# Kernel tuning notes

Hardware: AMD Instinct MI355X
Metric: run time of the kernel (lower is better)

Reference implementation:

```python
import jax, jax.numpy as jnp
import numpy as np

T, B, D, H = 2048, 2, 1024, 16
DPH = D // H
SCALE = DPH ** -0.5


def setup_inputs() -> dict:
    key = jax.random.key(0)
    ks = jax.random.split(key, 5)
    x = jax.random.normal(ks[0], (T, B, D), dtype=jnp.float32)
    Wk = jax.random.normal(ks[1], (D, D), dtype=jnp.float32) * 0.02
    Wv = jax.random.normal(ks[2], (D, D), dtype=jnp.float32) * 0.02
    Wq = jax.random.normal(ks[3], (D, D), dtype=jnp.float32) * 0.02
    Wo = jax.random.normal(ks[4], (D, D), dtype=jnp.float32) * 0.02
    # causal mask: True marks positions to hide (masked_fill semantics)
    mask = jnp.triu(jnp.ones((T, T), dtype=bool), k=1)
    return {"x": x, "Wk": Wk, "Wv": Wv, "Wq": Wq, "Wo": Wo, "mask": mask}


def _split_heads(y):
    # 't b (d h) -> b h t d' : d_per_head is the OUTER factor of the split
    t, b, _ = y.shape
    return y.reshape(t, b, DPH, H).transpose(1, 3, 0, 2)  # [b, h, t, d]


def reference(x, Wk, Wv, Wq, Wo, mask):
    # nn.Linear(bias=False): y = x @ W.T
    k = _split_heads(x @ Wk.T)
    v = _split_heads(x @ Wv.T)
    q = _split_heads(x @ Wq.T)
    scores = jnp.einsum('bhid,bhjd->bhij', q, k) * SCALE  # [b,h,t,t]
    scores = jnp.where(mask, -jnp.inf, scores)
    attn = jax.nn.softmax(scores, axis=-1)
    # dropout is identity in eval mode
    out = jnp.einsum('bhij,bhjd->bhid', attn, v)  # [b,h,t,d]
    # 'b h t d -> t b (h d)' : heads are the OUTER factor of the merge
    out = out.transpose(2, 0, 1, 3).reshape(x.shape[0], x.shape[1], D)
    return out @ Wo.T
```

## Files before the change

kernel.cpp:

```cpp
#include <hip/hip_runtime.h>

#define T_LEN   2048
#define BATCH   2
#define DMODEL  1024
#define NHEAD   16
#define DHEAD   64
#define MROWS   4096
#define KDIM    1024
#define NDIM    1024
#define ATT_SC2 (0.125f * 1.44269504088896f)

typedef unsigned short u16;
typedef unsigned int   u32;
typedef u16   u16x8 __attribute__((ext_vector_type(8)));
typedef u16   u16x4 __attribute__((ext_vector_type(4)));
typedef __bf16 bf16x8 __attribute__((ext_vector_type(8)));
typedef float f32x4 __attribute__((ext_vector_type(4)));

__device__ __forceinline__ u16 f2bf(float f) {
  u32 u = __builtin_bit_cast(u32, f);
  u += 0x7fffu + ((u >> 16) & 1u);
  return (u16)(u >> 16);
}

__device__ __forceinline__ u16 bfc(float f) {
  return __builtin_bit_cast(u16, (__bf16)f);
}

__device__ __forceinline__ f32x4 mfma16(u16x8 a, u16x8 b, f32x4 c) {
  return __builtin_amdgcn_mfma_f32_16x16x32_bf16(
      __builtin_bit_cast(bf16x8, a), __builtin_bit_cast(bf16x8, b), c, 0, 0, 0);
}

__device__ __forceinline__ void gload16(const u16* g, u16* l) {
  __builtin_amdgcn_global_load_lds((const __attribute__((address_space(1))) void*)g,
                                   (__attribute__((address_space(3))) void*)l,
                                   16, 0, 0);
}

#define XN 4194304u
__global__ __launch_bounds__(256) void cast_all(
    const float* __restrict__ x,  const float* __restrict__ wk,
    const float* __restrict__ wv, const float* __restrict__ wq,
    const float* __restrict__ wo, u16* __restrict__ ws) {
  size_t i = ((size_t)blockIdx.x * 256 + threadIdx.x) * 4;
  const float* src; size_t soff, doff; float sc = 1.0f;
  if (i < XN) {
    int m = (int)(i >> 10), d = (int)(i & 1023);
    int t = m >> 1, b = m & 1;
    src = x; soff = i;
    doff = ((size_t)(b * 2048 + t) << 10) + d;
  } else {
    size_t off = i - XN;
    int wi = (int)(off >> 20);
    off &= 1048575u;
    int u = (int)(off >> 10), c = (int)(off & 1023);
    src = (wi == 0) ? wk : (wi == 1) ? wv : (wi == 2) ? wq : wo;
    soff = off;
    if (wi == 3) {
      doff = XN + 3u * 1048576u + off;
    } else {
      int slot = (wi == 2) ? 0 : (wi == 0) ? 1 : 2;
      int up = (u & 15) * 64 + (u >> 4);
      doff = XN + (size_t)slot * 1048576u + ((size_t)up << 10) + c;
      if (wi == 2) sc = ATT_SC2;
    }
  }
  float4 v = *reinterpret_cast<const float4*>(src + soff);
  u16x4 o;
  o.s0 = f2bf(v.x * sc); o.s1 = f2bf(v.y * sc); o.s2 = f2bf(v.z * sc); o.s3 = f2bf(v.w * sc);
  *reinterpret_cast<u16x4*>(ws + doff) = o;
}

__global__ __launch_bounds__(256, 2) void gemm_qkv(
    const u16* __restrict__ xbm, const u16* __restrict__ Wqkv,
    u16* __restrict__ Qh, u16* __restrict__ Kh, u16* __restrict__ Vt) {
  __shared__ __align__(16) u16 As[256 * 64];
  __shared__ __align__(16) u16 Bs[128 * 64];

  const int tid = threadIdx.x;
  const int l  = tid & 63, w = tid >> 6;
  const int lr = l & 15,  lg = l >> 4;
  const int wm = w >> 1,  wn = w & 1;

  const int blk  = blockIdx.x;
  const int wgid = (blk & 7) * 48 + (blk >> 3);

  const u16 *A, *W;
  int m0, n0, isV;
  if (wgid < 256) {
    const int bx = wgid >> 4, by = wgid & 15;
    A = xbm; W = Wqkv; m0 = by * 256; n0 = bx * 128; isV = 0;
  } else {
    const int v = wgid - 256;
    const int vby = v >> 5, vbx = v & 31;
    A = Wqkv + (2048u << 10); W = xbm; m0 = vby * 256; n0 = vbx * 128; isV = 1;
  }

  f32x4 acc[8][4];
#pragma unroll
  for (int i = 0; i < 8; ++i)
#pragma unroll
    for (int j = 0; j < 4; ++j) acc[i][j] = (f32x4)(0.0f);

  for (int k0 = 0; k0 < KDIM; k0 += 64) {
#pragma unroll
    for (int i = 0; i < 8; ++i) {
      const int base = i * 256 + w * 64;
      const int p = base + l;
      const int r = p >> 3, c = p & 7;
      gload16(A + (size_t)(m0 + r) * KDIM + k0 + ((c ^ (r & 7)) << 3),
              As + (size_t)base * 8);
    }
#pragma unroll
    for (int i = 0; i < 4; ++i) {
      const int base = i * 256 + w * 64;
      const int p = base + l;
      const int r = p >> 3, c = p & 7;
      gload16(W + (size_t)(n0 + r) * KDIM + k0 + ((c ^ (r & 7)) << 3),
              Bs + (size_t)base * 8);
    }
    __syncthreads();

#pragma unroll
    for (int ks = 0; ks < 2; ++ks) {
      const int cr = ks * 4 + lg;
      u16x8 bf_[4];
#pragma unroll
      for (int ni = 0; ni < 4; ++ni) {
        const int rr = wn * 64 + ni * 16 + lr;
        bf_[ni] = *reinterpret_cast<const u16x8*>(Bs + rr * 64 + ((cr ^ (rr & 7)) << 3));
      }
      __builtin_amdgcn_s_setprio(1);
#pragma unroll
      for (int mi = 0; mi < 8; ++mi) {
        const int rr = wm * 128 + mi * 16 + lr;
        const u16x8 af = *reinterpret_cast<const u16x8*>(
            As + rr * 64 + ((cr ^ (rr & 7)) << 3));
#pragma unroll
        for (int ni = 0; ni < 4; ++ni)
          acc[mi][ni] = mfma16(af, bf_[ni], acc[mi][ni]);
      }
      __builtin_amdgcn_s_setprio(0);
    }
    __syncthreads();
  }

#pragma unroll
  for (int mi = 0; mi < 8; ++mi)
#pragma unroll
    for (int ni = 0; ni < 4; ++ni)
#pragma unroll
      for (int r = 0; r < 4; ++r) {
        const int row = m0 + wm * 128 + mi * 16 + lg * 4 + r;
        const int col = n0 + wn * 64 + ni * 16 + lr;
        const u16 v = bfc(acc[mi][ni][r]);
        if (!isV) {
          const int bb = row >> 11, t = row & 2047;
          const int c = col & 1023, hh = c >> 6, dp = c & 63;
          u16* d = (col < 1024) ? Qh : Kh;
          d[(((size_t)(bb * NHEAD + hh) << 11) + t) * 64 + dp] = v;
        } else {
          const int hh = row >> 6, dp = row & 63;
          const int bb = col >> 11, t = col & 2047;
          Vt[((((size_t)(bb * NHEAD + hh)) * 64 + dp) << 11) + t] = v;
        }
      }
}

__global__ __launch_bounds__(256) void gemm_o(
    const u16* __restrict__ A, const u16* __restrict__ W, float* __restrict__ out) {
  __shared__ __align__(16) u16 As[128 * 64];
  __shared__ __align__(16) u16 Bs[64 * 64];

  const int tid = threadIdx.x;
  const int l  = tid & 63, w = tid >> 6;
  const int lr = l & 15,  lg = l >> 4;
  const int wm = w >> 1,  wn = w & 1;

  const int blk  = blockIdx.x;
  const int wgid = (blk & 7) * 64 + (blk >> 3);
  const int bx = wgid >> 5, by = wgid & 31;
  const int m0 = by * 128;
  const int n0 = bx * 64;

  f32x4 acc[4][2];
#pragma unroll
  for (int i = 0; i < 4; ++i)
#pragma unroll
    for (int j = 0; j < 2; ++j) acc[i][j] = (f32x4)(0.0f);

  for (int k0 = 0; k0 < KDIM; k0 += 64) {
#pragma unroll
    for (int i = 0; i < 4; ++i) {
      const int base = i * 256 + w * 64;
      const int p = base + l;
      const int r = p >> 3, c = p & 7;
      gload16(A + (size_t)(m0 + r) * KDIM + k0 + ((c ^ (r & 7)) << 3),
              As + (size_t)base * 8);
    }
#pragma unroll
    for (int i = 0; i < 2; ++i) {
      const int base = i * 256 + w * 64;
      const int p = base + l;
      const int r = p >> 3, c = p & 7;
      gload16(W + (size_t)(n0 + r) * KDIM + k0 + ((c ^ (r & 7)) << 3),
              Bs + (size_t)base * 8);
    }
    __syncthreads();

#pragma unroll
    for (int ks = 0; ks < 2; ++ks) {
      const int cr = ks * 4 + lg;
      u16x8 bf_[2];
#pragma unroll
      for (int ni = 0; ni < 2; ++ni) {
        const int rr = wn * 32 + ni * 16 + lr;
        bf_[ni] = *reinterpret_cast<const u16x8*>(Bs + rr * 64 + ((cr ^ (rr & 7)) << 3));
      }
      __builtin_amdgcn_s_setprio(1);
#pragma unroll
      for (int mi = 0; mi < 4; ++mi) {
        const int rr = wm * 64 + mi * 16 + lr;
        const u16x8 af = *reinterpret_cast<const u16x8*>(
            As + rr * 64 + ((cr ^ (rr & 7)) << 3));
#pragma unroll
        for (int ni = 0; ni < 2; ++ni)
          acc[mi][ni] = mfma16(af, bf_[ni], acc[mi][ni]);
      }
      __builtin_amdgcn_s_setprio(0);
    }
    __syncthreads();
  }

#pragma unroll
  for (int mi = 0; mi < 4; ++mi)
#pragma unroll
    for (int ni = 0; ni < 2; ++ni)
#pragma unroll
      for (int r = 0; r < 4; ++r) {
        const int row = m0 + wm * 64 + mi * 16 + lg * 4 + r;
        const int col = n0 + wn * 32 + ni * 16 + lr;
        const int t = row & 2047, bb = row >> 11;
        out[((size_t)(t * 2 + bb) << 10) + col] = acc[mi][ni][r];
      }
}

__global__ __launch_bounds__(256) void attn_fwd(
    const u16* __restrict__ Qh, const u16* __restrict__ Kh,
    const u16* __restrict__ Vt, u16* __restrict__ Aout) {
  __shared__ __align__(16) u16 Ks[2][8192];
  __shared__ __align__(16) u16 Vs[2][8192];
  __shared__ __align__(16) u16 Pl[4][1024];

  const int tid = threadIdx.x;
  const int l = tid & 63, w = tid >> 6;
  const int lr = l & 15, lg = l >> 4;
  const int blk = blockIdx.x;
  const int bxx = (blk >> 3) & 15;
  const int bh  = ((blk >> 7) << 3) + (blk & 7);
  const int b = bh >> 4, h = bh & 15;

  const u16* kg = Kh + ((size_t)bh << 17);
  const u16* vg = Vt + ((size_t)bh << 17);

  const u16x8 ones = {0x3F80,0x3F80,0x3F80,0x3F80,0x3F80,0x3F80,0x3F80,0x3F80};

  auto stage = [&](int buf, int kv0) {
#pragma unroll
    for (int j = 0; j < 4; ++j) {
      const int base = (j * 4 + w) * 64;
      const int g = base + l;
      const int rk = g >> 3, ck = g & 7;
      gload16(kg + (size_t)(kv0 + rk) * 64 + ((ck ^ (rk & 7)) << 3),
              &Ks[buf][(size_t)base * 8]);
      const int rv = g >> 4, cv = g & 15;
      gload16(vg + ((size_t)rv << 11) + kv0 + ((cv ^ (rv & 15)) << 3),
              &Vs[buf][(size_t)base * 8]);
    }
  };

  for (int ph = 0; ph < 2; ++ph) {
    const int qb = ph ? bxx : 31 - bxx;
    const int qbase = qb * 64 + w * 16;
    const int qrow = qbase + lr;

    const u16* qptr = Qh + (((size_t)bh << 11) + qrow) * 64 + lg * 8;
    const u16x8 qf0 = *reinterpret_cast<const u16x8*>(qptr);
    const u16x8 qf1 = *reinterpret_cast<const u16x8*>(qptr + 32);

    f32x4 oacc[4];
#pragma unroll
    for (int i = 0; i < 4; ++i) oacc[i] = (f32x4)(0.0f);
    f32x4 sum4 = (f32x4)(0.0f);

    const int npair = (qb + 2) >> 1;
    stage(0, 0);
    __syncthreads();

    int cur = 0;
    for (int t = 0; t < npair; ++t) {
      const int kv0 = t * 128;
      if (t + 1 < npair) stage(cur ^ 1, kv0 + 128);

#pragma unroll
      for (int hh = 0; hh < 2; ++hh) {
        const int i64 = 2 * t + hh;
        if (i64 <= qb) {
          const bool diag = (i64 == qb);

          __builtin_amdgcn_s_setprio(1);
#pragma unroll
          for (int tt = 0; tt < 4; ++tt) {
            const int row = hh * 64 + tt * 16 + lr;
            const u16x8 kf0 = *reinterpret_cast<const u16x8*>(
                &Ks[cur][row * 64 + ((lg ^ (row & 7)) << 3)]);
            const u16x8 kf1 = *reinterpret_cast<const u16x8*>(
                &Ks[cur][row * 64 + (((4 + lg) ^ (row & 7)) << 3)]);
            f32x4 sacc = (f32x4)(0.0f);
            sacc = mfma16(kf0, qf0, sacc);
            sacc = mfma16(kf1, qf1, sacc);
            u16x4 pk;
#pragma unroll
            for (int r = 0; r < 4; ++r) {
              const int kv = kv0 + hh * 64 + tt * 16 + lg * 4 + r;
              const float s = (diag && kv > qrow) ? -1e30f : sacc[r];
              pk[r] = bfc(__builtin_amdgcn_exp2f(s - 8.0f));
            }
            *reinterpret_cast<u16x4*>(
                &Pl[w][lr * 64 + (((tt * 2 + (lg >> 1)) ^ (lr & 7)) << 3)
                       + ((lg & 1) << 2)]) = pk;
          }

#pragma unroll
          for (int kh = 0; kh < 2; ++kh) {
            const u16x8 pa = *reinterpret_cast<const u16x8*>(
                &Pl[w][lr * 64 + (((kh * 4 + lg) ^ (lr & 7)) << 3)]);
            sum4 = mfma16(pa, ones, sum4);
#pragma unroll
            for (int ni = 0; ni < 4; ++ni) {
              const int dr = ni * 16 + lr;
              const int ck = hh * 8 + kh * 4 + lg;
              const u16x8 vf = *reinterpret_cast<const u16x8*>(
                  &Vs[cur][dr * 128 + ((ck ^ (dr & 15)) << 3)]);
              oacc[ni] = mfma16(pa, vf, oacc[ni]);
            }
          }
          __builtin_amdgcn_s_setprio(0);
        }
      }

      __syncthreads();
      cur ^= 1;
    }

#pragma unroll
    for (int r = 0; r < 4; ++r) {
      const float inv = 1.0f / sum4[r];
      const int q = qbase + lg * 4 + r;
      const size_t rowbase = (((size_t)(b * 2048 + q)) << 10) + h * DHEAD;
#pragma unroll
      for (int ni = 0; ni < 4; ++ni)
        Aout[rowbase + ni * 16 + lr] = bfc(oacc[ni][r] * inv);
    }
  }
}

extern "C" void kernel_launch(void* const* d_in, const int* in_sizes, int n_in,
                              void* d_out, int out_size, void* d_ws, size_t ws_size,
                              hipStream_t stream) {
  const float* x  = (const float*)d_in[0];
  const float* Wk = (const float*)d_in[1];
  const float* Wv = (const float*)d_in[2];
  const float* Wq = (const float*)d_in[3];
  const float* Wo = (const float*)d_in[4];

  u16* ws   = (u16*)d_ws;
  u16* xbm  = ws;
  u16* Wqkv = xbm + 4194304;
  u16* Wob  = Wqkv + 3145728;
  u16* Qh   = Wob + 1048576;
  u16* Kh   = Qh  + 4194304;
  u16* Vt   = Kh  + 4194304;
  u16* Aout = Vt  + 4194304;

  cast_all<<<8192, 256, 0, stream>>>(x, Wk, Wv, Wq, Wo, ws);

  gemm_qkv<<<384, 256, 0, stream>>>(xbm, Wqkv, Qh, Kh, Vt);

  attn_fwd<<<512, 256, 0, stream>>>(Qh, Kh, Vt, Aout);

  gemm_o<<<512, 256, 0, stream>>>(Aout, Wob, (float*)d_out);
}
```

Baseline: 111.3 us.

## Split attention KV tiles across warps and reduce partial outputs via shared memory

The attention kernel now gives each warp a 32-row slice of the 128-row KV tile for all four 16-row query groups, instead of one query group over the whole KV tile. K and V fragments are loaded from LDS once per warp and reused across query groups, and fully masked groups are skipped per warp. Per-warp partial outputs and row sums are then combined through shared memory at the end. This adds a cross-warp reduction, an extra barrier and more accumulator registers, and sets launch_bounds to 2 blocks per CU.

Result: slower. 165.9 us (+49.0%).

```diff
diff --git a/kernel.cpp b/kernel.cpp
--- a/kernel.cpp
+++ b/kernel.cpp
@@ -246,12 +246,10 @@
       }
 }
 
-__global__ __launch_bounds__(256) void attn_fwd(
+__global__ __launch_bounds__(256, 2) void attn_fwd(
     const u16* __restrict__ Qh, const u16* __restrict__ Kh,
     const u16* __restrict__ Vt, u16* __restrict__ Aout) {
-  __shared__ __align__(16) u16 Ks[2][8192];
-  __shared__ __align__(16) u16 Vs[2][8192];
-  __shared__ __align__(16) u16 Pl[4][1024];
+  __shared__ __align__(16) u16 smem[34816];
 
   const int tid = threadIdx.x;
   const int l = tid & 63, w = tid >> 6;
@@ -263,36 +261,45 @@
 
   const u16* kg = Kh + ((size_t)bh << 17);
   const u16* vg = Vt + ((size_t)bh << 17);
+  u16* Pw = smem + 32768 + w * 512;
 
   const u16x8 ones = {0x3F80,0x3F80,0x3F80,0x3F80,0x3F80,0x3F80,0x3F80,0x3F80};
 
   auto stage = [&](int buf, int kv0) {
+    u16* kb = smem + buf * 8192;
+    u16* vb = smem + 16384 + buf * 8192;
 #pragma unroll
     for (int j = 0; j < 4; ++j) {
       const int base = (j * 4 + w) * 64;
       const int g = base + l;
       const int rk = g >> 3, ck = g & 7;
       gload16(kg + (size_t)(kv0 + rk) * 64 + ((ck ^ (rk & 7)) << 3),
-              &Ks[buf][(size_t)base * 8]);
+              kb + (size_t)base * 8);
       const int rv = g >> 4, cv = g & 15;
       gload16(vg + ((size_t)rv << 11) + kv0 + ((cv ^ (rv & 15)) << 3),
-              &Vs[buf][(size_t)base * 8]);
+              vb + (size_t)base * 8);
     }
   };
 
   for (int ph = 0; ph < 2; ++ph) {
     const int qb = ph ? bxx : 31 - bxx;
-    const int qbase = qb * 64 + w * 16;
-    const int qrow = qbase + lr;
-
-    const u16* qptr = Qh + (((size_t)bh << 11) + qrow) * 64 + lg * 8;
-    const u16x8 qf0 = *reinterpret_cast<const u16x8*>(qptr);
-    const u16x8 qf1 = *reinterpret_cast<const u16x8*>(qptr + 32);
-
-    f32x4 oacc[4];
-#pragma unroll
-    for (int i = 0; i < 4; ++i) oacc[i] = (f32x4)(0.0f);
-    f32x4 sum4 = (f32x4)(0.0f);
+    const int qmax = qb * 64 + 63;
+
+    u16x8 qf[4][2];
+#pragma unroll
+    for (int qg = 0; qg < 4; ++qg) {
+      const int qrow = qb * 64 + qg * 16 + lr;
+      const u16* qptr = Qh + (((size_t)bh << 11) + qrow) * 64 + lg * 8;
+      qf[qg][0] = *reinterpret_cast<const u16x8*>(qptr);
+      qf[qg][1] = *reinterpret_cast<const u16x8*>(qptr + 32);
+    }
+
+    f32x4 oacc[4][4];
+#pragma unroll
+    for (int qg = 0; qg < 4; ++qg)
+#pragma unroll
+      for (int i = 0; i < 4; ++i) oacc[qg][i] = (f32x4)(0.0f);
+    f32x4 sum4[4] = {(f32x4)(0.0f), (f32x4)(0.0f), (f32x4)(0.0f), (f32x4)(0.0f)};
 
     const int npair = (qb + 2) >> 1;
     stage(0, 0);
@@ -303,50 +310,73 @@
       const int kv0 = t * 128;
       if (t + 1 < npair) stage(cur ^ 1, kv0 + 128);
 
-#pragma unroll
-      for (int hh = 0; hh < 2; ++hh) {
-        const int i64 = 2 * t + hh;
-        if (i64 <= qb) {
-          const bool diag = (i64 == qb);
-
-          __builtin_amdgcn_s_setprio(1);
-#pragma unroll
-          for (int tt = 0; tt < 4; ++tt) {
-            const int row = hh * 64 + tt * 16 + lr;
-            const u16x8 kf0 = *reinterpret_cast<const u16x8*>(
-                &Ks[cur][row * 64 + ((lg ^ (row & 7)) << 3)]);
-            const u16x8 kf1 = *reinterpret_cast<const u16x8*>(
-                &Ks[cur][row * 64 + (((4 + lg) ^ (row & 7)) << 3)]);
-            f32x4 sacc = (f32x4)(0.0f);
-            sacc = mfma16(kf0, qf0, sacc);
-            sacc = mfma16(kf1, qf1, sacc);
-            u16x4 pk;
-#pragma unroll
-            for (int r = 0; r < 4; ++r) {
-              const int kv = kv0 + hh * 64 + tt * 16 + lg * 4 + r;
-              const float s = (diag && kv > qrow) ? -1e30f : sacc[r];
-              pk[r] = bfc(__builtin_amdgcn_exp2f(s - 8.0f));
+      const int kvw = kv0 + w * 32;
+      if (kvw <= qmax) {
+        const u16* kb = smem + cur * 8192;
+        const u16* vb = smem + 16384 + cur * 8192;
+
+        u16x8 kf[2][2];
+#pragma unroll
+        for (int tt = 0; tt < 2; ++tt) {
+          const int row = w * 32 + tt * 16 + lr;
+          kf[tt][0] = *reinterpret_cast<const u16x8*>(
+              kb + row * 64 + ((lg ^ (row & 7)) << 3));
+          kf[tt][1] = *reinterpret_cast<const u16x8*>(
+              kb + row * 64 + (((4 + lg) ^ (row & 7)) << 3));
+        }
+        u16x8 vf[4];
+#pragma unroll
+        for (int ni = 0; ni < 4; ++ni) {
+          const int dr = ni * 16 + lr;
+          const int ck = w * 4 + lg;
+          vf[ni] = *reinterpret_cast<const u16x8*>(
+              vb + dr * 128 + ((ck ^ (dr & 15)) << 3));
+        }
+
+#pragma unroll
+        for (int qg = 0; qg < 4; ++qg) {
+          const int qbg = qb * 64 + qg * 16;
+          if (kvw <= qbg + 15) {
+            f32x4 s0 = (f32x4)(0.0f), s1 = (f32x4)(0.0f);
+            __builtin_amdgcn_s_setprio(1);
+            s0 = mfma16(kf[0][0], qf[qg][0], s0);
+            s0 = mfma16(kf[0][1], qf[qg][1], s0);
+            s1 = mfma16(kf[1][0], qf[qg][0], s1);
+            s1 = mfma16(kf[1][1], qf[qg][1], s1);
+            __builtin_amdgcn_s_setprio(0);
+
+            const int qrow = qbg + lr;
+            u16x4 pk0, pk1;
+            if (kvw + 31 > qbg) {
+#pragma unroll
+              for (int r = 0; r < 4; ++r) {
+                const int kva = kvw + lg * 4 + r;
+                pk0[r] = bfc(__builtin_amdgcn_exp2f(
+                    (kva > qrow ? -1e30f : s0[r]) - 8.0f));
+                pk1[r] = bfc(__builtin_amdgcn_exp2f(
+                    (kva + 16 > qrow ? -1e30f : s1[r]) - 8.0f));
+              }
+            } else {
+#pragma unroll
+              for (int r = 0; r < 4; ++r) {
+                pk0[r] = bfc(__builtin_amdgcn_exp2f(s0[r] - 8.0f));
+                pk1[r] = bfc(__builtin_amdgcn_exp2f(s1[r] - 8.0f));
+              }
             }
-            *reinterpret_cast<u16x4*>(
-                &Pl[w][lr * 64 + (((tt * 2 + (lg >> 1)) ^ (lr & 7)) << 3)
-                       + ((lg & 1) << 2)]) = pk;
+            const int wo0 = lr * 32 + ((((lg >> 1)) ^ (lr & 3)) << 3) + ((lg & 1) << 2);
+            const int wo1 = lr * 32 + (((2 + (lg >> 1)) ^ (lr & 3)) << 3) + ((lg & 1) << 2);
+            *reinterpret_cast<u16x4*>(Pw + wo0) = pk0;
+            *reinterpret_cast<u16x4*>(Pw + wo1) = pk1;
+
+            const u16x8 pa = *reinterpret_cast<const u16x8*>(
+                Pw + lr * 32 + ((lg ^ (lr & 3)) << 3));
+            __builtin_amdgcn_s_setprio(1);
+            sum4[qg] = mfma16(pa, ones, sum4[qg]);
+#pragma unroll
+            for (int ni = 0; ni < 4; ++ni)
+              oacc[qg][ni] = mfma16(pa, vf[ni], oacc[qg][ni]);
+            __builtin_amdgcn_s_setprio(0);
           }
-
-#pragma unroll
-          for (int kh = 0; kh < 2; ++kh) {
-            const u16x8 pa = *reinterpret_cast<const u16x8*>(
-                &Pl[w][lr * 64 + (((kh * 4 + lg) ^ (lr & 7)) << 3)]);
-            sum4 = mfma16(pa, ones, sum4);
-#pragma unroll
-            for (int ni = 0; ni < 4; ++ni) {
-              const int dr = ni * 16 + lr;
-              const int ck = hh * 8 + kh * 4 + lg;
-              const u16x8 vf = *reinterpret_cast<const u16x8*>(
-                  &Vs[cur][dr * 128 + ((ck ^ (dr & 15)) << 3)]);
-              oacc[ni] = mfma16(pa, vf, oacc[ni]);
-            }
-          }
-          __builtin_amdgcn_s_setprio(0);
         }
       }
 
@@ -354,15 +384,54 @@
       cur ^= 1;
     }
 
+    float* red  = reinterpret_cast<float*>(smem);
+    float* sred = reinterpret_cast<float*>(smem + 32768);
+#pragma unroll
+    for (int qg = 0; qg < 4; ++qg) {
+      if (qg != w) {
+        float* p = red + (qg * 4 + w) * 1024;
+#pragma unroll
+        for (int ni = 0; ni < 4; ++ni)
+#pragma unroll
+          for (int r = 0; r < 4; ++r)
+            p[(lg * 4 + r) * 64 + ni * 16 + lr] = oacc[qg][ni][r];
+        if (lr == 0) {
+#pragma unroll
+          for (int r = 0; r < 4; ++r)
+            sred[(qg * 4 + w) * 16 + lg * 4 + r] = sum4[qg][r];
+        }
+      }
+    }
+    __syncthreads();
+
+    f32x4 o_[4]; f32x4 ss = sum4[w];
+#pragma unroll
+    for (int ni = 0; ni < 4; ++ni) o_[ni] = oacc[w][ni];
+#pragma unroll
+    for (int src = 0; src < 4; ++src) {
+      if (src != w) {
+        const float* p = red + (w * 4 + src) * 1024;
+#pragma unroll
+        for (int ni = 0; ni < 4; ++ni)
+#pragma unroll
+          for (int r = 0; r < 4; ++r)
+            o_[ni][r] += p[(lg * 4 + r) * 64 + ni * 16 + lr];
+#pragma unroll
+        for (int r = 0; r < 4; ++r)
+          ss[r] += sred[(w * 4 + src) * 16 + lg * 4 + r];
+      }
+    }
+
 #pragma unroll
     for (int r = 0; r < 4; ++r) {
-      const float inv = 1.0f / sum4[r];
-      const int q = qbase + lg * 4 + r;
+      const float inv = 1.0f / ss[r];
+      const int q = qb * 64 + w * 16 + lg * 4 + r;
       const size_t rowbase = (((size_t)(b * 2048 + q)) << 10) + h * DHEAD;
 #pragma unroll
       for (int ni = 0; ni < 4; ++ni)
-        Aout[rowbase + ni * 16 + lr] = bfc(oacc[ni][r] * inv);
-    }
+        Aout[rowbase + ni * 16 + lr] = bfc(o_[ni][r] * inv);
+    }
+    __syncthreads();
   }
 }
 
```

## Split attention KV tiles across two waves per query slice with LDS reduction

Applied to the files above, without the earlier changes.

The attention kernel moves from 4 to 8 waves per block. Each pair of waves shares a 16-row query slice and splits every 64-wide KV tile into two 32-column halves, and the partial outputs and row sums are combined through LDS at the end. The KV tile shrinks from 128 to 64 columns, so shared memory per block drops. Synchronization switches to explicit vmcnt/lgkmcnt waits with raw barriers, and V fragments are loaded before the MFMAs. This aims to raise occupancy and latency hiding, at the cost of more barriers per KV element and an extra reduction step.

Measured after the change: 107.8 us. -3.2%, faster.

```diff
diff --git a/kernel.cpp b/kernel.cpp
--- a/kernel.cpp
+++ b/kernel.cpp
@@ -246,16 +246,15 @@
       }
 }
 
-__global__ __launch_bounds__(256) void attn_fwd(
+__global__ __launch_bounds__(512, 2) void attn_fwd(
     const u16* __restrict__ Qh, const u16* __restrict__ Kh,
     const u16* __restrict__ Vt, u16* __restrict__ Aout) {
-  __shared__ __align__(16) u16 Ks[2][8192];
-  __shared__ __align__(16) u16 Vs[2][8192];
-  __shared__ __align__(16) u16 Pl[4][1024];
+  __shared__ __align__(16) u16 smem[20480];
 
   const int tid = threadIdx.x;
   const int l = tid & 63, w = tid >> 6;
   const int lr = l & 15, lg = l >> 4;
+  const int wk = w & 1, wq = w >> 1;
   const int blk = blockIdx.x;
   const int bxx = (blk >> 3) & 15;
   const int bh  = ((blk >> 7) << 3) + (blk & 7);
@@ -263,27 +262,27 @@
 
   const u16* kg = Kh + ((size_t)bh << 17);
   const u16* vg = Vt + ((size_t)bh << 17);
+  u16* Pw = smem + 16384 + w * 512;
+
+  float* redO = reinterpret_cast<float*>(smem);
+  float* redS = reinterpret_cast<float*>(smem + 16384);
 
   const u16x8 ones = {0x3F80,0x3F80,0x3F80,0x3F80,0x3F80,0x3F80,0x3F80,0x3F80};
 
   auto stage = [&](int buf, int kv0) {
-#pragma unroll
-    for (int j = 0; j < 4; ++j) {
-      const int base = (j * 4 + w) * 64;
-      const int g = base + l;
-      const int rk = g >> 3, ck = g & 7;
-      gload16(kg + (size_t)(kv0 + rk) * 64 + ((ck ^ (rk & 7)) << 3),
-              &Ks[buf][(size_t)base * 8]);
-      const int rv = g >> 4, cv = g & 15;
-      gload16(vg + ((size_t)rv << 11) + kv0 + ((cv ^ (rv & 15)) << 3),
-              &Vs[buf][(size_t)base * 8]);
-    }
+    u16* kb = smem + buf * 4096;
+    u16* vb = smem + 8192 + buf * 4096;
+    const int p = w * 64 + l;
+    const int r = p >> 3, c = p & 7;
+    const int cs = ((c ^ (r & 7)) << 3);
+    gload16(kg + (size_t)(kv0 + r) * 64 + cs, kb + (size_t)(w * 64) * 8);
+    gload16(vg + ((size_t)r << 11) + kv0 + cs, vb + (size_t)(w * 64) * 8);
   };
 
   for (int ph = 0; ph < 2; ++ph) {
     const int qb = ph ? bxx : 31 - bxx;
-    const int qbase = qb * 64 + w * 16;
-    const int qrow = qbase + lr;
+    const int qbw = qb * 64 + wq * 16;
+    const int qrow = qbw + lr;
 
     const u16* qptr = Qh + (((size_t)bh << 11) + qrow) * 64 + lg * 8;
     const u16x8 qf0 = *reinterpret_cast<const u16x8*>(qptr);
@@ -294,75 +293,116 @@
     for (int i = 0; i < 4; ++i) oacc[i] = (f32x4)(0.0f);
     f32x4 sum4 = (f32x4)(0.0f);
 
-    const int npair = (qb + 2) >> 1;
+    const int nt = qb + 1;
     stage(0, 0);
     __syncthreads();
 
     int cur = 0;
-    for (int t = 0; t < npair; ++t) {
-      const int kv0 = t * 128;
-      if (t + 1 < npair) stage(cur ^ 1, kv0 + 128);
-
-#pragma unroll
-      for (int hh = 0; hh < 2; ++hh) {
-        const int i64 = 2 * t + hh;
-        if (i64 <= qb) {
-          const bool diag = (i64 == qb);
-
-          __builtin_amdgcn_s_setprio(1);
-#pragma unroll
-          for (int tt = 0; tt < 4; ++tt) {
-            const int row = hh * 64 + tt * 16 + lr;
-            const u16x8 kf0 = *reinterpret_cast<const u16x8*>(
-                &Ks[cur][row * 64 + ((lg ^ (row & 7)) << 3)]);
-            const u16x8 kf1 = *reinterpret_cast<const u16x8*>(
-                &Ks[cur][row * 64 + (((4 + lg) ^ (row & 7)) << 3)]);
-            f32x4 sacc = (f32x4)(0.0f);
-            sacc = mfma16(kf0, qf0, sacc);
-            sacc = mfma16(kf1, qf1, sacc);
-            u16x4 pk;
-#pragma unroll
-            for (int r = 0; r < 4; ++r) {
-              const int kv = kv0 + hh * 64 + tt * 16 + lg * 4 + r;
-              const float s = (diag && kv > qrow) ? -1e30f : sacc[r];
-              pk[r] = bfc(__builtin_amdgcn_exp2f(s - 8.0f));
-            }
-            *reinterpret_cast<u16x4*>(
-                &Pl[w][lr * 64 + (((tt * 2 + (lg >> 1)) ^ (lr & 7)) << 3)
-                       + ((lg & 1) << 2)]) = pk;
+    for (int t = 0; t < nt; ++t) {
+      const int kv0 = t * 64;
+      const bool pf = (t + 1 < nt);
+      if (pf) {
+        stage(cur ^ 1, kv0 + 64);
+        asm volatile("s_waitcnt vmcnt(2)" ::: "memory");
+      } else {
+        asm volatile("s_waitcnt vmcnt(0)" ::: "memory");
+      }
+      __builtin_amdgcn_sched_barrier(0);
+      __builtin_amdgcn_s_barrier();
+
+      const int kvw = kv0 + wk * 32;
+      if (kvw <= qbw + 15) {
+        const u16* kb = smem + cur * 4096;
+        const u16* vb = smem + 8192 + cur * 4096;
+
+        u16x8 kf[2][2];
+#pragma unroll
+        for (int tt = 0; tt < 2; ++tt) {
+          const int row = wk * 32 + tt * 16 + lr;
+          kf[tt][0] = *reinterpret_cast<const u16x8*>(
+              kb + row * 64 + ((lg ^ (row & 7)) << 3));
+          kf[tt][1] = *reinterpret_cast<const u16x8*>(
+              kb + row * 64 + (((4 + lg) ^ (row & 7)) << 3));
+        }
+        u16x8 vf[4];
+#pragma unroll
+        for (int ni = 0; ni < 4; ++ni) {
+          const int dr = ni * 16 + lr;
+          const int ck = wk * 4 + lg;
+          vf[ni] = *reinterpret_cast<const u16x8*>(
+              vb + dr * 64 + ((ck ^ (dr & 7)) << 3));
+        }
+
+        const bool diag = (kvw + 31 > qbw);
+
+        __builtin_amdgcn_s_setprio(1);
+#pragma unroll
+        for (int tt = 0; tt < 2; ++tt) {
+          f32x4 sacc = (f32x4)(0.0f);
+          sacc = mfma16(kf[tt][0], qf0, sacc);
+          sacc = mfma16(kf[tt][1], qf1, sacc);
+          u16x4 pk;
+#pragma unroll
+          for (int r = 0; r < 4; ++r) {
+            const int kv = kvw + tt * 16 + lg * 4 + r;
+            const float s = (diag && kv > qrow) ? -1e30f : sacc[r];
+            pk[r] = bfc(__builtin_amdgcn_exp2f(s - 8.0f));
           }
-
-#pragma unroll
-          for (int kh = 0; kh < 2; ++kh) {
-            const u16x8 pa = *reinterpret_cast<const u16x8*>(
-                &Pl[w][lr * 64 + (((kh * 4 + lg) ^ (lr & 7)) << 3)]);
-            sum4 = mfma16(pa, ones, sum4);
-#pragma unroll
-            for (int ni = 0; ni < 4; ++ni) {
-              const int dr = ni * 16 + lr;
-              const int ck = hh * 8 + kh * 4 + lg;
-              const u16x8 vf = *reinterpret_cast<const u16x8*>(
-                  &Vs[cur][dr * 128 + ((ck ^ (dr & 15)) << 3)]);
-              oacc[ni] = mfma16(pa, vf, oacc[ni]);
-            }
-          }
-          __builtin_amdgcn_s_setprio(0);
+          *reinterpret_cast<u16x4*>(
+              &Pw[lr * 32 + (((tt * 2 + (lg >> 1)) ^ (lr & 3)) << 3)
+                  + ((lg & 1) << 2)]) = pk;
         }
-      }
-
-      __syncthreads();
+
+        {
+          const u16x8 pa = *reinterpret_cast<const u16x8*>(
+              &Pw[lr * 32 + ((lg ^ (lr & 3)) << 3)]);
+          sum4 = mfma16(pa, ones, sum4);
+#pragma unroll
+          for (int ni = 0; ni < 4; ++ni)
+            oacc[ni] = mfma16(pa, vf[ni], oacc[ni]);
+        }
+        __builtin_amdgcn_s_setprio(0);
+      }
+
+      asm volatile("s_waitcnt lgkmcnt(0)" ::: "memory");
+      __builtin_amdgcn_sched_barrier(0);
+      __builtin_amdgcn_s_barrier();
       cur ^= 1;
     }
 
-#pragma unroll
-    for (int r = 0; r < 4; ++r) {
-      const float inv = 1.0f / sum4[r];
-      const int q = qbase + lg * 4 + r;
-      const size_t rowbase = (((size_t)(b * 2048 + q)) << 10) + h * DHEAD;
+    if (wk) {
+      float* po = redO + wq * 1088;
 #pragma unroll
       for (int ni = 0; ni < 4; ++ni)
-        Aout[rowbase + ni * 16 + lr] = bfc(oacc[ni][r] * inv);
-    }
+#pragma unroll
+        for (int r = 0; r < 4; ++r)
+          po[(lg * 4 + r) * 68 + ni * 16 + lr] = oacc[ni][r];
+      if (lr == 0) {
+#pragma unroll
+        for (int r = 0; r < 4; ++r)
+          redS[wq * 16 + lg * 4 + r] = sum4[r];
+      }
+    }
+    __syncthreads();
+
+    if (!wk) {
+      const float* po = redO + wq * 1088;
+      f32x4 ss = sum4;
+#pragma unroll
+      for (int r = 0; r < 4; ++r)
+        ss[r] += redS[wq * 16 + lg * 4 + r];
+#pragma unroll
+      for (int r = 0; r < 4; ++r) {
+        const float inv = 1.0f / ss[r];
+        const int q = qbw + lg * 4 + r;
+        const size_t rowbase = (((size_t)(b * 2048 + q)) << 10) + h * DHEAD;
+#pragma unroll
+        for (int ni = 0; ni < 4; ++ni)
+          Aout[rowbase + ni * 16 + lr] = bfc(
+              (oacc[ni][r] + po[(lg * 4 + r) * 68 + ni * 16 + lr]) * inv);
+      }
+    }
+    __syncthreads();
   }
 }
 
@@ -388,7 +428,7 @@
 
   gemm_qkv<<<384, 256, 0, stream>>>(xbm, Wqkv, Qh, Kh, Vt);
 
-  attn_fwd<<<512, 256, 0, stream>>>(Qh, Kh, Vt, Aout);
+  attn_fwd<<<512, 512, 0, stream>>>(Qh, Kh, Vt, Aout);
 
   gemm_o<<<512, 256, 0, stream>>>(Aout, Wob, (float*)d_out);
 }
```
